# Optimization experiments

Measured on AMD Instinct MI355X. Metric: run time of the kernel, lower is better.

Reference implementation:

```python
import jax, jax.numpy as jnp
import numpy as np

DIMS = 1024
BATCH, SEQ = 4, 2048

def setup_inputs() -> dict:
    key = jax.random.key(0)
    k1, k2, k3, k4 = jax.random.split(key, 4)
    scale = 1.0 / np.sqrt(DIMS)
    return {
        "input_seq_embs": jax.random.normal(k1, (BATCH, SEQ, DIMS), dtype=jnp.float32),
        "Wq": jax.random.normal(k2, (DIMS, DIMS), dtype=jnp.float32) * scale,
        "Wk": jax.random.normal(k3, (DIMS, DIMS), dtype=jnp.float32) * scale,
        "Wv": jax.random.normal(k4, (DIMS, DIMS), dtype=jnp.float32) * scale,
    }

def reference(input_seq_embs, Wq, Wk, Wv):
    # nn.Linear(x) = x @ W.T ; weights stored [out, in]
    q = jnp.einsum('bsd,ed->bse', input_seq_embs, Wq)
    k = jnp.einsum('bsd,ed->bse', input_seq_embs, Wk)
    v = jnp.einsum('bsd,ed->bse', input_seq_embs, Wv)
    # full N x N scores, NO 1/sqrt(d) scaling (faithful to source)
    scores = jnp.einsum('bqe,bke->bqk', q, k)
    causal = jnp.tril(jnp.ones((q.shape[1], q.shape[1]), dtype=bool))
    scores = jnp.where(causal[None, :, :], scores, -jnp.inf)
    attn = jax.nn.softmax(scores, axis=-1)
    return jnp.einsum('bqk,bke->bqe', attn, v)
```

## Files before the change

kernel.cpp:

```cpp
#include <hip/hip_runtime.h>


typedef _Float16 h8 __attribute__((ext_vector_type(8)));
typedef float f32x4 __attribute__((ext_vector_type(4)));

#define BM 128
#define BN 128
#define BK 32

__device__ __forceinline__ void gl_lds16(const _Float16* g, _Float16* l) {
    __builtin_amdgcn_global_load_lds(
        (const __attribute__((address_space(1))) void*)g,
        (__attribute__((address_space(3))) void*)l, 16, 0, 0);
}

template<int SWZ, int OM, bool KLIM>
__global__ __launch_bounds__(256) void gemm_nt(
    const _Float16* __restrict__ A, const _Float16* __restrict__ B,
    void* __restrict__ Cp, int N, int K,
    size_t sAz, size_t sBz, size_t sCz)
{
    __shared__ _Float16 As[BM * BK];
    __shared__ _Float16 Bs[BN * BK];

    int bx, by;
    if (SWZ == 1) {
        const int r = blockIdx.x & 7, q2 = blockIdx.x >> 3;
        bx = q2 >> 3;
        by = ((q2 & 7) << 3) | r;
    } else if (SWZ == 2) {
        const int r = blockIdx.x & 7, g = blockIdx.x >> 3;
        if (g <= r) { by = r;      bx = g; }
        else        { by = 15 - r; bx = g - (r + 1); }
    } else if (SWZ == 3) {
        const int r = blockIdx.x & 7, g = blockIdx.x >> 3;
        by = (g & 1) ? (15 - r) : r;
        bx = g >> 1;
    } else {
        bx = blockIdx.x; by = blockIdx.y;
    }

    const int tid  = threadIdx.x;
    const int lane = tid & 63;
    const int wv   = tid >> 6;
    const int m0 = by * BM, n0 = bx * BN;
    const size_t z = blockIdx.z;

    const int lr = lane >> 2;
    const int lc = (lane & 3) * 8;
    const _Float16* pA0 = A + z * sAz + (size_t)(m0 + wv * 16 + lr) * K + lc;
    const _Float16* pA1 = pA0 + (size_t)64 * K;
    const _Float16* pB0 = B + z * sBz + (size_t)(n0 + wv * 16 + lr) * K + lc;
    const _Float16* pB1 = pB0 + (size_t)64 * K;
    _Float16* lA0 = As + wv * 512;
    _Float16* lA1 = As + (wv + 4) * 512;
    _Float16* lB0 = Bs + wv * 512;
    _Float16* lB1 = Bs + (wv + 4) * 512;

    const int la = lane & 15;
    const int qd = lane >> 4;
    const int wm = (wv >> 1) * 64;
    const int wn = (wv & 1) * 64;

    f32x4 acc[4][4];
    #pragma unroll
    for (int i = 0; i < 4; i++)
        #pragma unroll
        for (int j = 0; j < 4; j++)
            acc[i][j] = (f32x4){0.f, 0.f, 0.f, 0.f};

    const int kEnd = KLIM ? (m0 + BM) : K;

    for (int k0 = 0; k0 < kEnd; k0 += BK) {
        gl_lds16(pA0, lA0);
        gl_lds16(pA1, lA1);
        gl_lds16(pB0, lB0);
        gl_lds16(pB1, lB1);
        pA0 += BK; pA1 += BK; pB0 += BK; pB1 += BK;
        __syncthreads();

        h8 af[4], bf[4];
        #pragma unroll
        for (int i = 0; i < 4; i++)
            af[i] = *(const h8*)&As[(wm + i * 16 + la) * BK + qd * 8];
        #pragma unroll
        for (int i = 0; i < 4; i++)
            bf[i] = *(const h8*)&Bs[(wn + i * 16 + la) * BK + qd * 8];
        #pragma unroll
        for (int i = 0; i < 4; i++)
            #pragma unroll
            for (int j = 0; j < 4; j++)
                acc[i][j] = __builtin_amdgcn_mfma_f32_16x16x32_f16(af[i], bf[j], acc[i][j], 0, 0, 0);
        __syncthreads();
    }

    if (OM == 2) {
        _Float16* C = (_Float16*)Cp;
        #pragma unroll
        for (int i = 0; i < 4; i++)
            #pragma unroll
            for (int j = 0; j < 4; j++) {
                const int col  = n0 + wn + j * 16 + la;
                const size_t base = (size_t)(col >> 10) * 8388608 + (col & 1023);
                #pragma unroll
                for (int rr = 0; rr < 4; rr++)
                    C[base + (size_t)(m0 + wm + i * 16 + qd * 4 + rr) * 1024] =
                        (_Float16)acc[i][j][rr];
            }
    } else if (OM == 1) {
        _Float16* C = (_Float16*)Cp + z * sCz;
        #pragma unroll
        for (int i = 0; i < 4; i++)
            #pragma unroll
            for (int j = 0; j < 4; j++)
                #pragma unroll
                for (int rr = 0; rr < 4; rr++)
                    C[(size_t)(m0 + wm + i * 16 + qd * 4 + rr) * N + (n0 + wn + j * 16 + la)] =
                        (_Float16)acc[i][j][rr];
    } else {
        float* C = (float*)Cp + z * sCz;
        #pragma unroll
        for (int i = 0; i < 4; i++)
            #pragma unroll
            for (int j = 0; j < 4; j++)
                #pragma unroll
                for (int rr = 0; rr < 4; rr++)
                    C[(size_t)(m0 + wm + i * 16 + qd * 4 + rr) * N + (n0 + wn + j * 16 + la)] =
                        acc[i][j][rr];
    }
}

__global__ __launch_bounds__(256) void cvt8(const float* __restrict__ in,
                                            _Float16* __restrict__ out)
{
    const size_t i = ((size_t)blockIdx.x * 256 + threadIdx.x) * 8;
    float4 a = *(const float4*)(in + i);
    float4 b = *(const float4*)(in + i + 4);
    h8 o = { (_Float16)a.x, (_Float16)a.y, (_Float16)a.z, (_Float16)a.w,
             (_Float16)b.x, (_Float16)b.y, (_Float16)b.z, (_Float16)b.w };
    *(h8*)(out + i) = o;
}

__global__ __launch_bounds__(256) void cvt_w3(const float* __restrict__ Wq,
                                              const float* __restrict__ Wk,
                                              const float* __restrict__ Wv,
                                              _Float16* __restrict__ out)
{
    const int zz = blockIdx.y;
    const float* in = (zz == 0) ? Wq : ((zz == 1) ? Wk : Wv);
    const size_t i = ((size_t)blockIdx.x * 256 + threadIdx.x) * 8;
    float4 a = *(const float4*)(in + i);
    float4 b = *(const float4*)(in + i + 4);
    h8 o = { (_Float16)a.x, (_Float16)a.y, (_Float16)a.z, (_Float16)a.w,
             (_Float16)b.x, (_Float16)b.y, (_Float16)b.z, (_Float16)b.w };
    *(h8*)(out + (size_t)zz * 1048576 + i) = o;
}

__global__ __launch_bounds__(256) void softmax_causal(const float* __restrict__ S,
                                                      _Float16* __restrict__ P)
{
    const int idx = blockIdx.x;
    const int q = idx & 2047;
    const float* Srow = S + (size_t)idx * 2048;
    _Float16* Prow = P + (size_t)idx * 2048;
    const int t = threadIdx.x;
    const int lane = t & 63, wv = t >> 6;
    __shared__ float red[4];

    float vals[8];
    float mx = -3.4e38f;
    #pragma unroll
    for (int i = 0; i < 8; i++) {
        vals[i] = -3.4e38f;
        if (i * 256 <= q) {
            int k = t + i * 256;
            if (k <= q) vals[i] = Srow[k];
            mx = fmaxf(mx, vals[i]);
        }
    }
    #pragma unroll
    for (int o = 32; o > 0; o >>= 1) mx = fmaxf(mx, __shfl_down(mx, o, 64));
    if (lane == 0) red[wv] = mx;
    __syncthreads();
    const float mall = fmaxf(fmaxf(red[0], red[1]), fmaxf(red[2], red[3]));
    __syncthreads();

    float sum = 0.f;
    #pragma unroll
    for (int i = 0; i < 8; i++) {
        if (i * 256 <= q) {
            int k = t + i * 256;
            float e = (k <= q) ? __expf(vals[i] - mall) : 0.f;
            vals[i] = e;
            sum += e;
        } else vals[i] = 0.f;
    }
    #pragma unroll
    for (int o = 32; o > 0; o >>= 1) sum += __shfl_down(sum, o, 64);
    if (lane == 0) red[wv] = sum;
    __syncthreads();
    const float inv = 1.f / (red[0] + red[1] + red[2] + red[3]);

    const int kceil = ((q >> 7) + 1) << 7;
    #pragma unroll
    for (int i = 0; i < 8; i++) {
        if (i * 256 >= kceil) break;
        int k = t + i * 256;
        if (k < kceil) Prow[k] = (_Float16)(vals[i] * inv);
    }
}

__global__ __launch_bounds__(256) void transpose_v_kernel(const _Float16* __restrict__ V,
                                                          _Float16* __restrict__ Vt)
{
    __shared__ _Float16 tile[64][72];
    const int b = blockIdx.z;
    const int s0 = blockIdx.x * 64;
    const int e0 = blockIdx.y * 64;
    const _Float16* Vb = V + (size_t)b * 2048 * 1024;
    _Float16* Vtb = Vt + (size_t)b * 1024 * 2048;
    const int r = threadIdx.x >> 2;
    const int c = (threadIdx.x & 3) * 16;

    const _Float16* src = &Vb[(size_t)(s0 + r) * 1024 + e0 + c];
    *(uint4*)&tile[r][c]     = *(const uint4*)src;
    *(uint4*)&tile[r][c + 8] = *(const uint4*)(src + 8);
    __syncthreads();

    h8 o0, o1;
    #pragma unroll
    for (int j = 0; j < 8; j++) o0[j] = tile[c + j][r];
    #pragma unroll
    for (int j = 0; j < 8; j++) o1[j] = tile[c + 8 + j][r];
    _Float16* dst = &Vtb[(size_t)(e0 + r) * 2048 + s0 + c];
    *(h8*)dst       = o0;
    *(h8*)(dst + 8) = o1;
}

extern "C" void kernel_launch(void* const* d_in, const int* in_sizes, int n_in,
                              void* d_out, int out_size, void* d_ws, size_t ws_size,
                              hipStream_t stream) {
    const float* x  = (const float*)d_in[0];
    const float* Wq = (const float*)d_in[1];
    const float* Wk = (const float*)d_in[2];
    const float* Wv = (const float*)d_in[3];
    float* out = (float*)d_out;

    const size_t MiB = 1024 * 1024;
    char* ws = (char*)d_ws;
    _Float16* QKVh = (_Float16*)ws;
    _Float16* Vh   = QKVh + (size_t)2 * 8388608;
    float*    S    = (float*)(ws + 48 * MiB);
    _Float16* x_h  = (_Float16*)(ws + 48 * MiB);
    _Float16* Wh   = (_Float16*)(ws + 64 * MiB);
    _Float16* P    = (_Float16*)ws;
    _Float16* Vt   = (_Float16*)(ws + 48 * MiB);

    const dim3 blk(256);

    cvt8<<<dim3(4096), blk, 0, stream>>>(x, x_h);
    cvt_w3<<<dim3(512, 3), blk, 0, stream>>>(Wq, Wk, Wv, Wh);

    gemm_nt<1, 2, false><<<dim3(1536), blk, 0, stream>>>(
        x_h, Wh, QKVh, 3072, 1024, 0, 0, 0);

    gemm_nt<2, 0, false><<<dim3(136, 1, 4), blk, 0, stream>>>(
        QKVh, QKVh + 8388608, S, 2048, 1024,
        (size_t)2097152, (size_t)2097152, (size_t)4194304);

    softmax_causal<<<dim3(4 * 2048), blk, 0, stream>>>(S, P);

    transpose_v_kernel<<<dim3(32, 16, 4), blk, 0, stream>>>(Vh, Vt);

    gemm_nt<3, 0, true><<<dim3(128, 1, 4), blk, 0, stream>>>(
        P, Vt, out, 1024, 2048,
        (size_t)4194304, (size_t)2097152, (size_t)2097152);
}
```

Measured before the change: 283.3 us.

## Stage GEMM epilogues through LDS, vectorize softmax, merge conversion kernels

The GEMM epilogues now write accumulators into swizzled shared memory and then store them to global memory as 16-byte vectors, replacing scattered scalar stores. The softmax kernel gives each thread 8 contiguous elements, so it can use float4 loads and an h8 store. The two fp32-to-fp16 conversion kernels become a single launch. The aim is better store coalescing and less launch overhead, paid for with extra barriers and an LDS round trip in the epilogue.

```diff
diff --git a/kernel.cpp b/kernel.cpp
--- a/kernel.cpp
+++ b/kernel.cpp
@@ -20,8 +20,9 @@
     void* __restrict__ Cp, int N, int K,
     size_t sAz, size_t sBz, size_t sCz)
 {
-    __shared__ _Float16 As[BM * BK];
-    __shared__ _Float16 Bs[BN * BK];
+    __shared__ __align__(16) char smem[16384];
+    _Float16* As = (_Float16*)smem;
+    _Float16* Bs = (_Float16*)(smem + 8192);
 
     int bx, by;
     if (SWZ == 1) {
@@ -95,65 +96,93 @@
     }
 
     if (OM == 2) {
-        _Float16* C = (_Float16*)Cp;
-        #pragma unroll
-        for (int i = 0; i < 4; i++)
+        _Float16* H = (_Float16*)smem;
+        #pragma unroll
+        for (int h = 0; h < 2; h++) {
+            __syncthreads();
+            if ((wn >> 6) == h) {
+                #pragma unroll
+                for (int j = 0; j < 4; j++) {
+                    const int col = j * 16 + la;
+                    #pragma unroll
+                    for (int i = 0; i < 4; i++)
+                        #pragma unroll
+                        for (int rr = 0; rr < 4; rr++) {
+                            const int row = wm + i * 16 + qd * 4 + rr;
+                            H[row * 64 + ((((col >> 3) ^ (row & 7)) << 3) | (col & 7))] =
+                                (_Float16)acc[i][j][rr];
+                        }
+                }
+            }
+            __syncthreads();
+            const int row = tid >> 1;
+            const int cb  = (tid & 1) * 32;
+            const int gcol = n0 + h * 64 + cb;
+            _Float16* C = (_Float16*)Cp + (size_t)(gcol >> 10) * 8388608
+                        + (size_t)(m0 + row) * 1024 + (gcol & 1023);
             #pragma unroll
-            for (int j = 0; j < 4; j++) {
-                const int col  = n0 + wn + j * 16 + la;
-                const size_t base = (size_t)(col >> 10) * 8388608 + (col & 1023);
+            for (int gi = 0; gi < 4; gi++) {
+                const int col = cb + gi * 8;
+                h8 vv = *(const h8*)&H[row * 64 + (((col >> 3) ^ (row & 7)) << 3)];
+                *(h8*)(C + gi * 8) = vv;
+            }
+        }
+    } else {
+        float* R = (float*)smem;
+        #pragma unroll
+        for (int q4 = 0; q4 < 4; q4++) {
+            __syncthreads();
+            if ((wn >> 6) == (q4 >> 1)) {
+                const int jj = (q4 & 1) * 2;
                 #pragma unroll
-                for (int rr = 0; rr < 4; rr++)
-                    C[base + (size_t)(m0 + wm + i * 16 + qd * 4 + rr) * 1024] =
-                        (_Float16)acc[i][j][rr];
+                for (int jd = 0; jd < 2; jd++) {
+                    const int col = jd * 16 + la;
+                    #pragma unroll
+                    for (int i = 0; i < 4; i++)
+                        #pragma unroll
+                        for (int rr = 0; rr < 4; rr++) {
+                            const int row = wm + i * 16 + qd * 4 + rr;
+                            R[row * 32 + ((((col >> 2) ^ (row & 7)) << 2) | (col & 3))] =
+                                acc[i][jj + jd][rr];
+                        }
+                }
             }
-    } else if (OM == 1) {
-        _Float16* C = (_Float16*)Cp + z * sCz;
-        #pragma unroll
-        for (int i = 0; i < 4; i++)
+            __syncthreads();
+            const int row = tid >> 1;
+            const int cb  = (tid & 1) * 16;
+            float* C = (float*)Cp + z * sCz + (size_t)(m0 + row) * N + n0 + q4 * 32 + cb;
             #pragma unroll
-            for (int j = 0; j < 4; j++)
-                #pragma unroll
-                for (int rr = 0; rr < 4; rr++)
-                    C[(size_t)(m0 + wm + i * 16 + qd * 4 + rr) * N + (n0 + wn + j * 16 + la)] =
-                        (_Float16)acc[i][j][rr];
+            for (int gi = 0; gi < 4; gi++) {
+                const int col = cb + gi * 4;
+                f32x4 vv = *(const f32x4*)&R[row * 32 + (((col >> 2) ^ (row & 7)) << 2)];
+                *(f32x4*)(C + gi * 4) = vv;
+            }
+        }
+    }
+}
+
+__global__ __launch_bounds__(256) void cvt_all(
+    const float* __restrict__ x, const float* __restrict__ Wq,
+    const float* __restrict__ Wk, const float* __restrict__ Wv,
+    _Float16* __restrict__ x_h, _Float16* __restrict__ Wh)
+{
+    const int bid = blockIdx.x;
+    const float* src; _Float16* dst; size_t off;
+    if (bid < 4096) {
+        src = x; dst = x_h; off = (size_t)bid * 2048;
     } else {
-        float* C = (float*)Cp + z * sCz;
-        #pragma unroll
-        for (int i = 0; i < 4; i++)
-            #pragma unroll
-            for (int j = 0; j < 4; j++)
-                #pragma unroll
-                for (int rr = 0; rr < 4; rr++)
-                    C[(size_t)(m0 + wm + i * 16 + qd * 4 + rr) * N + (n0 + wn + j * 16 + la)] =
-                        acc[i][j][rr];
-    }
-}
-
-__global__ __launch_bounds__(256) void cvt8(const float* __restrict__ in,
-                                            _Float16* __restrict__ out)
-{
-    const size_t i = ((size_t)blockIdx.x * 256 + threadIdx.x) * 8;
-    float4 a = *(const float4*)(in + i);
-    float4 b = *(const float4*)(in + i + 4);
+        const int b2 = bid - 4096;
+        const int w = b2 >> 9;
+        src = (w == 0) ? Wq : ((w == 1) ? Wk : Wv);
+        dst = Wh + (size_t)w * 1048576;
+        off = (size_t)(b2 & 511) * 2048;
+    }
+    const size_t i = off + (size_t)threadIdx.x * 8;
+    float4 a = *(const float4*)(src + i);
+    float4 b = *(const float4*)(src + i + 4);
     h8 o = { (_Float16)a.x, (_Float16)a.y, (_Float16)a.z, (_Float16)a.w,
              (_Float16)b.x, (_Float16)b.y, (_Float16)b.z, (_Float16)b.w };
-    *(h8*)(out + i) = o;
-}
-
-__global__ __launch_bounds__(256) void cvt_w3(const float* __restrict__ Wq,
-                                              const float* __restrict__ Wk,
-                                              const float* __restrict__ Wv,
-                                              _Float16* __restrict__ out)
-{
-    const int zz = blockIdx.y;
-    const float* in = (zz == 0) ? Wq : ((zz == 1) ? Wk : Wv);
-    const size_t i = ((size_t)blockIdx.x * 256 + threadIdx.x) * 8;
-    float4 a = *(const float4*)(in + i);
-    float4 b = *(const float4*)(in + i + 4);
-    h8 o = { (_Float16)a.x, (_Float16)a.y, (_Float16)a.z, (_Float16)a.w,
-             (_Float16)b.x, (_Float16)b.y, (_Float16)b.z, (_Float16)b.w };
-    *(h8*)(out + (size_t)zz * 1048576 + i) = o;
+    *(h8*)(dst + i) = o;
 }
 
 __global__ __launch_bounds__(256) void softmax_causal(const float* __restrict__ S,
@@ -164,20 +193,22 @@
     const float* Srow = S + (size_t)idx * 2048;
     _Float16* Prow = P + (size_t)idx * 2048;
     const int t = threadIdx.x;
+    const int k0 = t * 8;
     const int lane = t & 63, wv = t >> 6;
     __shared__ float red[4];
 
-    float vals[8];
+    float v[8];
+    const bool any = (k0 <= q);
+    if (any) {
+        float4 a = *(const float4*)(Srow + k0);
+        float4 b = *(const float4*)(Srow + k0 + 4);
+        v[0] = a.x; v[1] = a.y; v[2] = a.z; v[3] = a.w;
+        v[4] = b.x; v[5] = b.y; v[6] = b.z; v[7] = b.w;
+    }
     float mx = -3.4e38f;
     #pragma unroll
-    for (int i = 0; i < 8; i++) {
-        vals[i] = -3.4e38f;
-        if (i * 256 <= q) {
-            int k = t + i * 256;
-            if (k <= q) vals[i] = Srow[k];
-            mx = fmaxf(mx, vals[i]);
-        }
-    }
+    for (int j = 0; j < 8; j++)
+        if (any && k0 + j <= q) mx = fmaxf(mx, v[j]);
     #pragma unroll
     for (int o = 32; o > 0; o >>= 1) mx = fmaxf(mx, __shfl_down(mx, o, 64));
     if (lane == 0) red[wv] = mx;
@@ -187,13 +218,10 @@
 
     float sum = 0.f;
     #pragma unroll
-    for (int i = 0; i < 8; i++) {
-        if (i * 256 <= q) {
-            int k = t + i * 256;
-            float e = (k <= q) ? __expf(vals[i] - mall) : 0.f;
-            vals[i] = e;
-            sum += e;
-        } else vals[i] = 0.f;
+    for (int j = 0; j < 8; j++) {
+        float e = (any && k0 + j <= q) ? __expf(v[j] - mall) : 0.f;
+        v[j] = e;
+        sum += e;
     }
     #pragma unroll
     for (int o = 32; o > 0; o >>= 1) sum += __shfl_down(sum, o, 64);
@@ -202,11 +230,12 @@
     const float inv = 1.f / (red[0] + red[1] + red[2] + red[3]);
 
     const int kceil = ((q >> 7) + 1) << 7;
-    #pragma unroll
-    for (int i = 0; i < 8; i++) {
-        if (i * 256 >= kceil) break;
-        int k = t + i * 256;
-        if (k < kceil) Prow[k] = (_Float16)(vals[i] * inv);
+    if (k0 < kceil) {
+        h8 o = { (_Float16)(v[0] * inv), (_Float16)(v[1] * inv),
+                 (_Float16)(v[2] * inv), (_Float16)(v[3] * inv),
+                 (_Float16)(v[4] * inv), (_Float16)(v[5] * inv),
+                 (_Float16)(v[6] * inv), (_Float16)(v[7] * inv) };
+        *(h8*)(Prow + k0) = o;
     }
 }
 
@@ -258,8 +287,7 @@
 
     const dim3 blk(256);
 
-    cvt8<<<dim3(4096), blk, 0, stream>>>(x, x_h);
-    cvt_w3<<<dim3(512, 3), blk, 0, stream>>>(Wq, Wk, Wv, Wh);
+    cvt_all<<<dim3(5632), blk, 0, stream>>>(x, Wq, Wk, Wv, x_h, Wh);
 
     gemm_nt<1, 2, false><<<dim3(1536), blk, 0, stream>>>(
         x_h, Wh, QKVh, 3072, 1024, 0, 0, 0);
```

Measured after the change: 309.7 us. +9.3%, slower.
